# Performance work log

Measured on AMD Instinct MI355X. Metric: run time of the kernel, lower is better.

## Reference

```python
import jax, jax.numpy as jnp
import numpy as np

COMMITMENT_COST = 0.25
NUM_EMBEDDINGS = 512
EMBEDDING_DIM = 64


def setup_inputs() -> dict:
    key = jax.random.key(0)
    k1, k2 = jax.random.split(key)
    inputs = jax.random.normal(k1, (64, EMBEDDING_DIM, 32, 32), dtype=jnp.float32)
    # nn.Embedding init: uniform(-1/K, 1/K)
    emb_w = jax.random.uniform(
        k2, (NUM_EMBEDDINGS, EMBEDDING_DIM), dtype=jnp.float32,
        minval=-1.0 / NUM_EMBEDDINGS, maxval=1.0 / NUM_EMBEDDINGS)
    return {"inputs": inputs, "emb_w": emb_w}


def reference(inputs, emb_w):
    sg = jax.lax.stop_gradient
    # NCHW -> NHWC
    x = jnp.transpose(inputs, (0, 2, 3, 1))          # [B, H, W, D]
    B, H, W, D = x.shape
    flat = x.reshape(-1, D)                          # [N, D]
    dist = (jnp.sum(flat * flat, axis=1, keepdims=True)
            + jnp.sum(emb_w * emb_w, axis=1)
            - 2.0 * jnp.dot(flat, emb_w.T))          # [N, K]
    idx = jnp.argmin(dist, axis=1)                   # [N]
    # one-hot @ emb_w is just a gather
    quantized = emb_w[idx].reshape(B, H, W, D)       # [B, H, W, D]
    e_latent_loss = jnp.mean((sg(quantized) - x) ** 2)
    q_latent_loss = jnp.mean((quantized - sg(x)) ** 2)
    loss = q_latent_loss + COMMITMENT_COST * e_latent_loss
    # straight-through estimator
    quantized_st = x + sg(quantized - x)
    out = jnp.transpose(quantized_st, (0, 3, 1, 2))  # back to NCHW
    return loss, out, idx[:, None]
```

## Files before the change

kernel.cpp:

```cpp
#include <hip/hip_runtime.h>


#define D_     64
#define HW_    1024
#define N_     65536
#define K_     512
#define M_     128
#define CH_    128
#define NCH_   4
#define WCODES 32
#define NDTOT  (N_ * D_)

__global__ __launch_bounds__(256, 2) void vq_fused_kernel(const float* __restrict__ inp,
                                                          const float* __restrict__ emb,
                                                          float* __restrict__ out) {
    __shared__ float ebuf[CH_ * D_];
    __shared__ float ldsn[K_];
    __shared__ float sv[4 * M_];
    __shared__ int   si[4 * M_];
    __shared__ int   fi[M_];

    const int tid  = threadIdx.x;
    const int lane = tid & 63;
    const int w    = tid >> 6;
    const int n0   = blockIdx.x * M_;
    const int b    = n0 >> 10;
    const int hw0  = n0 & 1023;
    const float* xbase = inp + b * (D_ * HW_) + hw0;

#pragma unroll
    for (int i = 0; i < 8; ++i) {
        int q  = i * 256 + tid;
        int d  = q >> 5;
        int pq = q & 31;
        float4 v = *(const float4*)(xbase + d * HW_ + pq * 4);
        *(float4*)(ebuf + d * M_ + pq * 4) = v;
    }

#pragma unroll
    for (int c = 0; c < 2; ++c) {
        const int k = c * 256 + tid;
        const float* e = emb + k * D_;
        float el[64];
#pragma unroll
        for (int q = 0; q < 16; ++q) {
            float4 v = *(const float4*)(e + q * 4);
            el[4 * q + 0] = v.x; el[4 * q + 1] = v.y;
            el[4 * q + 2] = v.z; el[4 * q + 3] = v.w;
        }
        float r[8];
#pragma unroll
        for (int j = 0; j < 8; ++j) r[j] = __fmul_rn(el[j], el[j]);
#pragma unroll
        for (int i = 1; i < 8; ++i)
#pragma unroll
            for (int j = 0; j < 8; ++j)
                r[j] = __fadd_rn(r[j], __fmul_rn(el[i * 8 + j], el[i * 8 + j]));
        ldsn[k] = __fadd_rn(__fadd_rn(__fadd_rn(r[0], r[1]), __fadd_rn(r[2], r[3])),
                            __fadd_rn(__fadd_rn(r[4], r[5]), __fadd_rn(r[6], r[7])));
    }
    __syncthreads();

    float x0[64], x1[64];
#pragma unroll
    for (int d = 0; d < 64; ++d) {
        float2 v = *(const float2*)(ebuf + d * M_ + 2 * lane);
        x0[d] = v.x; x1[d] = v.y;
    }

    float r0[8], r1[8];
#pragma unroll
    for (int j = 0; j < 8; ++j) {
        r0[j] = __fmul_rn(x0[j], x0[j]);
        r1[j] = __fmul_rn(x1[j], x1[j]);
    }
#pragma unroll
    for (int i = 1; i < 8; ++i)
#pragma unroll
        for (int j = 0; j < 8; ++j) {
            r0[j] = __fadd_rn(r0[j], __fmul_rn(x0[i * 8 + j], x0[i * 8 + j]));
            r1[j] = __fadd_rn(r1[j], __fmul_rn(x1[i * 8 + j], x1[i * 8 + j]));
        }
    const float sx0 = __fadd_rn(__fadd_rn(__fadd_rn(r0[0], r0[1]), __fadd_rn(r0[2], r0[3])),
                                __fadd_rn(__fadd_rn(r0[4], r0[5]), __fadd_rn(r0[6], r0[7])));
    const float sx1 = __fadd_rn(__fadd_rn(__fadd_rn(r1[0], r1[1]), __fadd_rn(r1[2], r1[3])),
                                __fadd_rn(__fadd_rn(r1[4], r1[5]), __fadd_rn(r1[6], r1[7])));

    float runv0 = 3.4e38f, runv1 = 3.4e38f;
    int   runi0 = 0,       runi1 = 0;

    for (int c = 0; c < NCH_; ++c) {
        __syncthreads();
        const float4* src = (const float4*)(emb + c * (CH_ * D_));
        float4* dst = (float4*)ebuf;
#pragma unroll
        for (int i = 0; i < 8; ++i) {
            int q = i * 256 + tid;
            dst[q] = src[q];
        }
        __syncthreads();

        const int kbase = c * CH_ + w * WCODES;
        const float* ew = ebuf + (w * WCODES) * D_;
#pragma unroll 2
        for (int kk = 0; kk < WCODES; ++kk) {
            const float* ek = ew + kk * D_;
            const float nk = ldsn[kbase + kk];
            float acc0 = 0.f, acc1 = 0.f;
#pragma unroll
            for (int q = 0; q < 16; ++q) {
                float4 ev = *(const float4*)(ek + q * 4);
                acc0 = fmaf(x0[4 * q + 0], ev.x, acc0); acc1 = fmaf(x1[4 * q + 0], ev.x, acc1);
                acc0 = fmaf(x0[4 * q + 1], ev.y, acc0); acc1 = fmaf(x1[4 * q + 1], ev.y, acc1);
                acc0 = fmaf(x0[4 * q + 2], ev.z, acc0); acc1 = fmaf(x1[4 * q + 2], ev.z, acc1);
                acc0 = fmaf(x0[4 * q + 3], ev.w, acc0); acc1 = fmaf(x1[4 * q + 3], ev.w, acc1);
            }
            float t0 = __fadd_rn(sx0, nk);
            float v0 = __fadd_rn(t0, -2.0f * acc0);
            if (v0 < runv0) { runv0 = v0; runi0 = kbase + kk; }
            float t1 = __fadd_rn(sx1, nk);
            float v1 = __fadd_rn(t1, -2.0f * acc1);
            if (v1 < runv1) { runv1 = v1; runi1 = kbase + kk; }
        }
    }

    {
        const int p0 = 2 * lane, p1 = 2 * lane + 1;
        sv[w * M_ + p0] = runv0; si[w * M_ + p0] = runi0;
        sv[w * M_ + p1] = runv1; si[w * M_ + p1] = runi1;
    }
    __syncthreads();
    if (tid < M_) {
        float bv = 3.4e38f; int bi = 0x7fffffff;
#pragma unroll
        for (int g = 0; g < 4; ++g) {
            float v  = sv[g * M_ + tid];
            int   ii = si[g * M_ + tid];
            if (v < bv || (v == bv && ii < bi)) { bv = v; bi = ii; }
        }
        fi[tid] = bi;
        out[1 + NDTOT + n0 + tid] = (float)bi;
    }
    __syncthreads();

    if (w == 0) {
        const int i0 = fi[2 * lane], i1 = fi[2 * lane + 1];
        const float* e0 = emb + i0 * D_;
        const float* e1 = emb + i1 * D_;
        float local = 0.f;
#pragma unroll
        for (int q = 0; q < 16; ++q) {
            float4 a0 = *(const float4*)(e0 + 4 * q);
            float4 a1 = *(const float4*)(e1 + 4 * q);
            float d00 = a0.x - x0[4 * q + 0]; local = fmaf(d00, d00, local);
            float d01 = a0.y - x0[4 * q + 1]; local = fmaf(d01, d01, local);
            float d02 = a0.z - x0[4 * q + 2]; local = fmaf(d02, d02, local);
            float d03 = a0.w - x0[4 * q + 3]; local = fmaf(d03, d03, local);
            float d10 = a1.x - x1[4 * q + 0]; local = fmaf(d10, d10, local);
            float d11 = a1.y - x1[4 * q + 1]; local = fmaf(d11, d11, local);
            float d12 = a1.z - x1[4 * q + 2]; local = fmaf(d12, d12, local);
            float d13 = a1.w - x1[4 * q + 3]; local = fmaf(d13, d13, local);
        }
#pragma unroll
        for (int off = 32; off > 0; off >>= 1)
            local += __shfl_down(local, off, 64);
        if (lane == 0)
            atomicAdd(out, local * (1.25f / (float)NDTOT));
    }

    float* obase = out + 1 + b * (D_ * HW_) + hw0;
    for (int i = 0; i < 32; ++i) {
        int q = i * 256 + tid;
        int d = q >> 7;
        int p = q & 127;
        obase[d * HW_ + p] = emb[fi[p] * D_ + d];
    }
}

extern "C" void kernel_launch(void* const* d_in, const int* in_sizes, int n_in,
                              void* d_out, int out_size, void* d_ws, size_t ws_size,
                              hipStream_t stream) {
    const float* inp = (const float*)d_in[0];
    const float* emb = (const float*)d_in[1];
    float* out = (float*)d_out;
    (void)d_ws; (void)ws_size;

    hipMemsetAsync(d_out, 0, sizeof(float), stream);
    vq_fused_kernel<<<512, 256, 0, stream>>>(inp, emb, out);
}
```

Measured before the change: 154.1 us.

## Stream codebook through scalar loads instead of LDS staging, drop LDS x tile

The codebook is no longer staged through shared memory in chunks. Each wave now reads its own 128 codes directly into SGPRs with inline s_load_dwordx16 and feeds them as scalar operands to the FMAs, which removes the chunk barriers and LDS reads. Inputs are loaded straight from global memory into registers, skipping the LDS transpose. The output gather is reworked so each thread loads a contiguous half-row of its code with vector loads before the strided stores. The risks are a full lgkmcnt wait on every code with no overlap, heavy SGPR pressure, and the loss of reuse across waves, since each wave now scans a different quarter of the codebook.

```diff
diff --git a/kernel.cpp b/kernel.cpp
--- a/kernel.cpp
+++ b/kernel.cpp
@@ -1,20 +1,19 @@
 #include <hip/hip_runtime.h>
 
+
+typedef float f32x16 __attribute__((ext_vector_type(16)));
 
 #define D_     64
 #define HW_    1024
 #define N_     65536
 #define K_     512
 #define M_     128
-#define CH_    128
-#define NCH_   4
-#define WCODES 32
+#define WCODES 128
 #define NDTOT  (N_ * D_)
 
 __global__ __launch_bounds__(256, 2) void vq_fused_kernel(const float* __restrict__ inp,
                                                           const float* __restrict__ emb,
                                                           float* __restrict__ out) {
-    __shared__ float ebuf[CH_ * D_];
     __shared__ float ldsn[K_];
     __shared__ float sv[4 * M_];
     __shared__ int   si[4 * M_];
@@ -26,16 +25,16 @@
     const int n0   = blockIdx.x * M_;
     const int b    = n0 >> 10;
     const int hw0  = n0 & 1023;
-    const float* xbase = inp + b * (D_ * HW_) + hw0;
 
+    const float* xb = inp + b * (D_ * HW_) + hw0 + 2 * lane;
+    float x0[64], x1[64];
 #pragma unroll
-    for (int i = 0; i < 8; ++i) {
-        int q  = i * 256 + tid;
-        int d  = q >> 5;
-        int pq = q & 31;
-        float4 v = *(const float4*)(xbase + d * HW_ + pq * 4);
-        *(float4*)(ebuf + d * M_ + pq * 4) = v;
+    for (int d = 0; d < 64; ++d) {
+        float2 v = *(const float2*)(xb + d * HW_);
+        x0[d] = v.x; x1[d] = v.y;
     }
+#pragma unroll
+    for (int d = 0; d < 64; ++d) asm volatile("" : "+v"(x0[d]), "+v"(x1[d]));
 
 #pragma unroll
     for (int c = 0; c < 2; ++c) {
@@ -59,14 +58,6 @@
         ldsn[k] = __fadd_rn(__fadd_rn(__fadd_rn(r[0], r[1]), __fadd_rn(r[2], r[3])),
                             __fadd_rn(__fadd_rn(r[4], r[5]), __fadd_rn(r[6], r[7])));
     }
-    __syncthreads();
-
-    float x0[64], x1[64];
-#pragma unroll
-    for (int d = 0; d < 64; ++d) {
-        float2 v = *(const float2*)(ebuf + d * M_ + 2 * lane);
-        x0[d] = v.x; x1[d] = v.y;
-    }
 
     float r0[8], r1[8];
 #pragma unroll
@@ -85,47 +76,56 @@
                                 __fadd_rn(__fadd_rn(r0[4], r0[5]), __fadd_rn(r0[6], r0[7])));
     const float sx1 = __fadd_rn(__fadd_rn(__fadd_rn(r1[0], r1[1]), __fadd_rn(r1[2], r1[3])),
                                 __fadd_rn(__fadd_rn(r1[4], r1[5]), __fadd_rn(r1[6], r1[7])));
+    __syncthreads();
 
     float runv0 = 3.4e38f, runv1 = 3.4e38f;
     int   runi0 = 0,       runi1 = 0;
+    const int kb = __builtin_amdgcn_readfirstlane(w << 7);
+    const float* ew = emb + (size_t)kb * D_;
 
-    for (int c = 0; c < NCH_; ++c) {
-        __syncthreads();
-        const float4* src = (const float4*)(emb + c * (CH_ * D_));
-        float4* dst = (float4*)ebuf;
+    for (int kk = 0; kk < WCODES; ++kk) {
+        const float* ek = ew + kk * D_;
+        f32x16 e0, e1, e2, e3;
+        asm volatile(
+            "s_load_dwordx16 %0, %4, 0x0\n\t"
+            "s_load_dwordx16 %1, %4, 0x40\n\t"
+            "s_load_dwordx16 %2, %4, 0x80\n\t"
+            "s_load_dwordx16 %3, %4, 0xc0\n\t"
+            "s_waitcnt lgkmcnt(0)"
+            : "=s"(e0), "=s"(e1), "=s"(e2), "=s"(e3)
+            : "s"(ek));
+        const float nk = ldsn[kb + kk];
+        float acc0 = 0.f, acc1 = 0.f;
 #pragma unroll
-        for (int i = 0; i < 8; ++i) {
-            int q = i * 256 + tid;
-            dst[q] = src[q];
+        for (int j = 0; j < 16; ++j) {
+            acc0 = fmaf(x0[j], e0[j], acc0);
+            acc1 = fmaf(x1[j], e0[j], acc1);
         }
-        __syncthreads();
-
-        const int kbase = c * CH_ + w * WCODES;
-        const float* ew = ebuf + (w * WCODES) * D_;
-#pragma unroll 2
-        for (int kk = 0; kk < WCODES; ++kk) {
-            const float* ek = ew + kk * D_;
-            const float nk = ldsn[kbase + kk];
-            float acc0 = 0.f, acc1 = 0.f;
 #pragma unroll
-            for (int q = 0; q < 16; ++q) {
-                float4 ev = *(const float4*)(ek + q * 4);
-                acc0 = fmaf(x0[4 * q + 0], ev.x, acc0); acc1 = fmaf(x1[4 * q + 0], ev.x, acc1);
-                acc0 = fmaf(x0[4 * q + 1], ev.y, acc0); acc1 = fmaf(x1[4 * q + 1], ev.y, acc1);
-                acc0 = fmaf(x0[4 * q + 2], ev.z, acc0); acc1 = fmaf(x1[4 * q + 2], ev.z, acc1);
-                acc0 = fmaf(x0[4 * q + 3], ev.w, acc0); acc1 = fmaf(x1[4 * q + 3], ev.w, acc1);
-            }
-            float t0 = __fadd_rn(sx0, nk);
-            float v0 = __fadd_rn(t0, -2.0f * acc0);
-            if (v0 < runv0) { runv0 = v0; runi0 = kbase + kk; }
-            float t1 = __fadd_rn(sx1, nk);
-            float v1 = __fadd_rn(t1, -2.0f * acc1);
-            if (v1 < runv1) { runv1 = v1; runi1 = kbase + kk; }
+        for (int j = 0; j < 16; ++j) {
+            acc0 = fmaf(x0[16 + j], e1[j], acc0);
+            acc1 = fmaf(x1[16 + j], e1[j], acc1);
         }
+#pragma unroll
+        for (int j = 0; j < 16; ++j) {
+            acc0 = fmaf(x0[32 + j], e2[j], acc0);
+            acc1 = fmaf(x1[32 + j], e2[j], acc1);
+        }
+#pragma unroll
+        for (int j = 0; j < 16; ++j) {
+            acc0 = fmaf(x0[48 + j], e3[j], acc0);
+            acc1 = fmaf(x1[48 + j], e3[j], acc1);
+        }
+        float t0 = __fadd_rn(sx0, nk);
+        float v0 = __fadd_rn(t0, -2.0f * acc0);
+        if (v0 < runv0) { runv0 = v0; runi0 = kb + kk; }
+        float t1 = __fadd_rn(sx1, nk);
+        float v1 = __fadd_rn(t1, -2.0f * acc1);
+        if (v1 < runv1) { runv1 = v1; runi1 = kb + kk; }
     }
 
     {
-        const int p0 = 2 * lane, p1 = 2 * lane + 1;
+        const int p0 = 2 * lane, p1 = p0 + 1;
         sv[w * M_ + p0] = runv0; si[w * M_ + p0] = runi0;
         sv[w * M_ + p1] = runv1; si[w * M_ + p1] = runi1;
     }
@@ -145,13 +145,13 @@
 
     if (w == 0) {
         const int i0 = fi[2 * lane], i1 = fi[2 * lane + 1];
-        const float* e0 = emb + i0 * D_;
-        const float* e1 = emb + i1 * D_;
+        const float* e0p = emb + i0 * D_;
+        const float* e1p = emb + i1 * D_;
         float local = 0.f;
 #pragma unroll
         for (int q = 0; q < 16; ++q) {
-            float4 a0 = *(const float4*)(e0 + 4 * q);
-            float4 a1 = *(const float4*)(e1 + 4 * q);
+            float4 a0 = *(const float4*)(e0p + 4 * q);
+            float4 a1 = *(const float4*)(e1p + 4 * q);
             float d00 = a0.x - x0[4 * q + 0]; local = fmaf(d00, d00, local);
             float d01 = a0.y - x0[4 * q + 1]; local = fmaf(d01, d01, local);
             float d02 = a0.z - x0[4 * q + 2]; local = fmaf(d02, d02, local);
@@ -168,12 +168,21 @@
             atomicAdd(out, local * (1.25f / (float)NDTOT));
     }
 
-    float* obase = out + 1 + b * (D_ * HW_) + hw0;
-    for (int i = 0; i < 32; ++i) {
-        int q = i * 256 + tid;
-        int d = q >> 7;
-        int p = q & 127;
-        obase[d * HW_ + p] = emb[fi[p] * D_ + d];
+    {
+        const int p     = tid & 127;
+        const int dhalf = tid >> 7;
+        const float* er = emb + fi[p] * D_ + dhalf * 32;
+        float ev[32];
+#pragma unroll
+        for (int q = 0; q < 8; ++q) {
+            float4 v = *(const float4*)(er + 4 * q);
+            ev[4 * q + 0] = v.x; ev[4 * q + 1] = v.y;
+            ev[4 * q + 2] = v.z; ev[4 * q + 3] = v.w;
+        }
+        float* ob = out + 1 + b * (D_ * HW_) + hw0 + p;
+#pragma unroll
+        for (int dd = 0; dd < 32; ++dd)
+            ob[(dhalf * 32 + dd) * HW_] = ev[dd];
     }
 }
 
```

New measurement: 138.1 us. 1.12x faster.

## Register-tile the distance GEMM with a 16x8 outer-product per thread

Applied to the files above, without the earlier changes.

Replaces the per-thread two-point dot-product loop with a register-blocked outer product: each thread accumulates 16 points by 8 codes over D, reading x and transposed codebook tiles from padded LDS. The codebook is loaded into LDS in two 256-code transposed chunks instead of four 128-code chunks, and the argmin reduction now merges 32 partial columns per point. The epilogue loss and output write are spread across all 256 threads, with a shared-memory partial sum. The cost is a large LDS footprint and about 128 accumulator registers per thread, so occupancy drops to one block per SIMD group (launch_bounds 256,1).

```diff
diff --git a/kernel.cpp b/kernel.cpp
--- a/kernel.cpp
+++ b/kernel.cpp
@@ -6,23 +6,25 @@
 #define N_     65536
 #define K_     512
 #define M_     128
-#define CH_    128
-#define NCH_   4
-#define WCODES 32
 #define NDTOT  (N_ * D_)
-
-__global__ __launch_bounds__(256, 2) void vq_fused_kernel(const float* __restrict__ inp,
+#define XP     160
+#define EP     256
+
+__global__ __launch_bounds__(256, 1) void vq_fused_kernel(const float* __restrict__ inp,
                                                           const float* __restrict__ emb,
                                                           float* __restrict__ out) {
-    __shared__ float ebuf[CH_ * D_];
+    __shared__ float ldsx[D_ * XP];
+    __shared__ float ldse[D_ * EP];
     __shared__ float ldsn[K_];
-    __shared__ float sv[4 * M_];
-    __shared__ int   si[4 * M_];
+    __shared__ float sxs[M_];
     __shared__ int   fi[M_];
+    __shared__ float psum[256];
 
     const int tid  = threadIdx.x;
     const int lane = tid & 63;
     const int w    = tid >> 6;
+    const int pg   = lane & 7;
+    const int kg   = lane >> 3;
     const int n0   = blockIdx.x * M_;
     const int b    = n0 >> 10;
     const int hw0  = n0 & 1023;
@@ -30,13 +32,12 @@
 
 #pragma unroll
     for (int i = 0; i < 8; ++i) {
-        int q  = i * 256 + tid;
-        int d  = q >> 5;
+        int q = i * 256 + tid;
+        int d = q >> 5;
         int pq = q & 31;
         float4 v = *(const float4*)(xbase + d * HW_ + pq * 4);
-        *(float4*)(ebuf + d * M_ + pq * 4) = v;
-    }
-
+        *(float4*)(ldsx + d * XP + (pq >> 2) * 20 + (pq & 3) * 4) = v;
+    }
 #pragma unroll
     for (int c = 0; c < 2; ++c) {
         const int k = c * 256 + tid;
@@ -59,83 +60,131 @@
         ldsn[k] = __fadd_rn(__fadd_rn(__fadd_rn(r[0], r[1]), __fadd_rn(r[2], r[3])),
                             __fadd_rn(__fadd_rn(r[4], r[5]), __fadd_rn(r[6], r[7])));
     }
-    __syncthreads();
-
-    float x0[64], x1[64];
-#pragma unroll
-    for (int d = 0; d < 64; ++d) {
-        float2 v = *(const float2*)(ebuf + d * M_ + 2 * lane);
-        x0[d] = v.x; x1[d] = v.y;
-    }
-
-    float r0[8], r1[8];
-#pragma unroll
-    for (int j = 0; j < 8; ++j) {
-        r0[j] = __fmul_rn(x0[j], x0[j]);
-        r1[j] = __fmul_rn(x1[j], x1[j]);
-    }
-#pragma unroll
-    for (int i = 1; i < 8; ++i)
+#pragma unroll
+    for (int i = 0; i < 16; ++i) {
+        float4 v = *(const float4*)(emb + tid * D_ + i * 4);
+        ldse[(i * 4 + 0) * EP + tid] = v.x;
+        ldse[(i * 4 + 1) * EP + tid] = v.y;
+        ldse[(i * 4 + 2) * EP + tid] = v.z;
+        ldse[(i * 4 + 3) * EP + tid] = v.w;
+    }
+    __syncthreads();
+
+    if (tid < M_) {
+        const int xb2 = (tid >> 4) * 20 + (tid & 15);
+        float r[8];
 #pragma unroll
         for (int j = 0; j < 8; ++j) {
-            r0[j] = __fadd_rn(r0[j], __fmul_rn(x0[i * 8 + j], x0[i * 8 + j]));
-            r1[j] = __fadd_rn(r1[j], __fmul_rn(x1[i * 8 + j], x1[i * 8 + j]));
-        }
-    const float sx0 = __fadd_rn(__fadd_rn(__fadd_rn(r0[0], r0[1]), __fadd_rn(r0[2], r0[3])),
-                                __fadd_rn(__fadd_rn(r0[4], r0[5]), __fadd_rn(r0[6], r0[7])));
-    const float sx1 = __fadd_rn(__fadd_rn(__fadd_rn(r1[0], r1[1]), __fadd_rn(r1[2], r1[3])),
-                                __fadd_rn(__fadd_rn(r1[4], r1[5]), __fadd_rn(r1[6], r1[7])));
-
-    float runv0 = 3.4e38f, runv1 = 3.4e38f;
-    int   runi0 = 0,       runi1 = 0;
-
-    for (int c = 0; c < NCH_; ++c) {
-        __syncthreads();
-        const float4* src = (const float4*)(emb + c * (CH_ * D_));
-        float4* dst = (float4*)ebuf;
-#pragma unroll
-        for (int i = 0; i < 8; ++i) {
-            int q = i * 256 + tid;
-            dst[q] = src[q];
-        }
-        __syncthreads();
-
-        const int kbase = c * CH_ + w * WCODES;
-        const float* ew = ebuf + (w * WCODES) * D_;
-#pragma unroll 2
-        for (int kk = 0; kk < WCODES; ++kk) {
-            const float* ek = ew + kk * D_;
-            const float nk = ldsn[kbase + kk];
-            float acc0 = 0.f, acc1 = 0.f;
-#pragma unroll
-            for (int q = 0; q < 16; ++q) {
-                float4 ev = *(const float4*)(ek + q * 4);
-                acc0 = fmaf(x0[4 * q + 0], ev.x, acc0); acc1 = fmaf(x1[4 * q + 0], ev.x, acc1);
-                acc0 = fmaf(x0[4 * q + 1], ev.y, acc0); acc1 = fmaf(x1[4 * q + 1], ev.y, acc1);
-                acc0 = fmaf(x0[4 * q + 2], ev.z, acc0); acc1 = fmaf(x1[4 * q + 2], ev.z, acc1);
-                acc0 = fmaf(x0[4 * q + 3], ev.w, acc0); acc1 = fmaf(x1[4 * q + 3], ev.w, acc1);
+            float v = ldsx[j * XP + xb2];
+            r[j] = __fmul_rn(v, v);
+        }
+#pragma unroll
+        for (int i = 1; i < 8; ++i)
+#pragma unroll
+            for (int j = 0; j < 8; ++j) {
+                float v = ldsx[(i * 8 + j) * XP + xb2];
+                r[j] = __fadd_rn(r[j], __fmul_rn(v, v));
             }
-            float t0 = __fadd_rn(sx0, nk);
-            float v0 = __fadd_rn(t0, -2.0f * acc0);
-            if (v0 < runv0) { runv0 = v0; runi0 = kbase + kk; }
-            float t1 = __fadd_rn(sx1, nk);
-            float v1 = __fadd_rn(t1, -2.0f * acc1);
-            if (v1 < runv1) { runv1 = v1; runi1 = kbase + kk; }
-        }
-    }
-
+        sxs[tid] = __fadd_rn(__fadd_rn(__fadd_rn(r[0], r[1]), __fadd_rn(r[2], r[3])),
+                             __fadd_rn(__fadd_rn(r[4], r[5]), __fadd_rn(r[6], r[7])));
+    }
+    __syncthreads();
+
+    float sxp[16];
     {
-        const int p0 = 2 * lane, p1 = 2 * lane + 1;
-        sv[w * M_ + p0] = runv0; si[w * M_ + p0] = runi0;
-        sv[w * M_ + p1] = runv1; si[w * M_ + p1] = runi1;
+        float4 s0 = *(const float4*)(sxs + pg * 16);
+        float4 s1 = *(const float4*)(sxs + pg * 16 + 4);
+        float4 s2 = *(const float4*)(sxs + pg * 16 + 8);
+        float4 s3 = *(const float4*)(sxs + pg * 16 + 12);
+        sxp[0]=s0.x; sxp[1]=s0.y; sxp[2]=s0.z; sxp[3]=s0.w;
+        sxp[4]=s1.x; sxp[5]=s1.y; sxp[6]=s1.z; sxp[7]=s1.w;
+        sxp[8]=s2.x; sxp[9]=s2.y; sxp[10]=s2.z; sxp[11]=s2.w;
+        sxp[12]=s3.x; sxp[13]=s3.y; sxp[14]=s3.z; sxp[15]=s3.w;
+    }
+    float runv[16];
+    int   runi[16];
+#pragma unroll
+    for (int j = 0; j < 16; ++j) { runv[j] = 3.4e38f; runi[j] = 0; }
+
+#pragma unroll 1
+    for (int c = 0; c < 2; ++c) {
+        if (c) {
+            __syncthreads();
+#pragma unroll
+            for (int i = 0; i < 16; ++i) {
+                float4 v = *(const float4*)(emb + (256 + tid) * D_ + i * 4);
+                ldse[(i * 4 + 0) * EP + tid] = v.x;
+                ldse[(i * 4 + 1) * EP + tid] = v.y;
+                ldse[(i * 4 + 2) * EP + tid] = v.z;
+                ldse[(i * 4 + 3) * EP + tid] = v.w;
+            }
+            __syncthreads();
+        }
+        float nk[8];
+        {
+            float4 na = *(const float4*)(ldsn + c * 256 + w * 64 + kg * 8);
+            float4 nb = *(const float4*)(ldsn + c * 256 + w * 64 + kg * 8 + 4);
+            nk[0]=na.x; nk[1]=na.y; nk[2]=na.z; nk[3]=na.w;
+            nk[4]=nb.x; nk[5]=nb.y; nk[6]=nb.z; nk[7]=nb.w;
+        }
+        float acc[16][8];
+#pragma unroll
+        for (int j = 0; j < 16; ++j)
+#pragma unroll
+            for (int q = 0; q < 8; ++q) acc[j][q] = 0.f;
+
+        const float* xcol = ldsx + pg * 20;
+        const float* ecol = ldse + (w << 6) + (kg << 3);
+#pragma unroll 4
+        for (int d = 0; d < 64; ++d) {
+            const float* xr = xcol + d * XP;
+            float4 xa = *(const float4*)(xr);
+            float4 xb4 = *(const float4*)(xr + 4);
+            float4 xc4 = *(const float4*)(xr + 8);
+            float4 xd4 = *(const float4*)(xr + 12);
+            const float* er = ecol + d * EP;
+            float4 ea = *(const float4*)(er);
+            float4 eb = *(const float4*)(er + 4);
+            float xv[16] = {xa.x, xa.y, xa.z, xa.w, xb4.x, xb4.y, xb4.z, xb4.w,
+                            xc4.x, xc4.y, xc4.z, xc4.w, xd4.x, xd4.y, xd4.z, xd4.w};
+            float ev[8]  = {ea.x, ea.y, ea.z, ea.w, eb.x, eb.y, eb.z, eb.w};
+#pragma unroll
+            for (int j = 0; j < 16; ++j)
+#pragma unroll
+                for (int q = 0; q < 8; ++q)
+                    acc[j][q] = fmaf(xv[j], ev[q], acc[j][q]);
+        }
+
+        const int kidx0 = c * 256 + w * 64 + kg * 8;
+#pragma unroll
+        for (int j = 0; j < 16; ++j) {
+            float sx = sxp[j];
+#pragma unroll
+            for (int q = 0; q < 8; ++q) {
+                float t = __fadd_rn(sx, nk[q]);
+                float v = __fadd_rn(t, -2.0f * acc[j][q]);
+                if (v < runv[j]) { runv[j] = v; runi[j] = kidx0 + q; }
+            }
+        }
+    }
+
+    __syncthreads();
+    float* mv = ldse;
+    int*   mi = (int*)(ldse + 128 * 33);
+    const int col = w * 8 + kg;
+#pragma unroll
+    for (int j = 0; j < 16; ++j) {
+        int p = pg * 16 + j;
+        mv[p * 33 + col] = runv[j];
+        mi[p * 33 + col] = runi[j];
     }
     __syncthreads();
     if (tid < M_) {
         float bv = 3.4e38f; int bi = 0x7fffffff;
 #pragma unroll
-        for (int g = 0; g < 4; ++g) {
-            float v  = sv[g * M_ + tid];
-            int   ii = si[g * M_ + tid];
+        for (int g = 0; g < 32; ++g) {
+            float v  = mv[tid * 33 + g];
+            int   ii = mi[tid * 33 + g];
             if (v < bv || (v == bv && ii < bi)) { bv = v; bi = ii; }
         }
         fi[tid] = bi;
@@ -143,37 +192,37 @@
     }
     __syncthreads();
 
-    if (w == 0) {
-        const int i0 = fi[2 * lane], i1 = fi[2 * lane + 1];
-        const float* e0 = emb + i0 * D_;
-        const float* e1 = emb + i1 * D_;
+    {
+        const int p  = tid & 127;
+        const int dh = tid >> 7;
+        const float* er2 = emb + fi[p] * D_ + dh * 32;
+        float ev2[32];
+#pragma unroll
+        for (int q = 0; q < 8; ++q) {
+            float4 v = *(const float4*)(er2 + 4 * q);
+            ev2[4 * q + 0] = v.x; ev2[4 * q + 1] = v.y;
+            ev2[4 * q + 2] = v.z; ev2[4 * q + 3] = v.w;
+        }
+        float* ob = out + 1 + b * (D_ * HW_) + hw0 + p;
+        const int xb2 = (p >> 4) * 20 + (p & 15);
         float local = 0.f;
 #pragma unroll
-        for (int q = 0; q < 16; ++q) {
-            float4 a0 = *(const float4*)(e0 + 4 * q);
-            float4 a1 = *(const float4*)(e1 + 4 * q);
-            float d00 = a0.x - x0[4 * q + 0]; local = fmaf(d00, d00, local);
-            float d01 = a0.y - x0[4 * q + 1]; local = fmaf(d01, d01, local);
-            float d02 = a0.z - x0[4 * q + 2]; local = fmaf(d02, d02, local);
-            float d03 = a0.w - x0[4 * q + 3]; local = fmaf(d03, d03, local);
-            float d10 = a1.x - x1[4 * q + 0]; local = fmaf(d10, d10, local);
-            float d11 = a1.y - x1[4 * q + 1]; local = fmaf(d11, d11, local);
-            float d12 = a1.z - x1[4 * q + 2]; local = fmaf(d12, d12, local);
-            float d13 = a1.w - x1[4 * q + 3]; local = fmaf(d13, d13, local);
-        }
+        for (int dd = 0; dd < 32; ++dd) {
+            float xv = ldsx[(dh * 32 + dd) * XP + xb2];
+            float df = ev2[dd] - xv;
+            local = fmaf(df, df, local);
+            ob[(dh * 32 + dd) * HW_] = ev2[dd];
+        }
+        psum[tid] = local;
+    }
+    __syncthreads();
+    if (tid < 64) {
+        float s = psum[tid] + psum[tid + 64] + psum[tid + 128] + psum[tid + 192];
 #pragma unroll
         for (int off = 32; off > 0; off >>= 1)
-            local += __shfl_down(local, off, 64);
-        if (lane == 0)
-            atomicAdd(out, local * (1.25f / (float)NDTOT));
-    }
-
-    float* obase = out + 1 + b * (D_ * HW_) + hw0;
-    for (int i = 0; i < 32; ++i) {
-        int q = i * 256 + tid;
-        int d = q >> 7;
-        int p = q & 127;
-        obase[d * HW_ + p] = emb[fi[p] * D_ + d];
+            s += __shfl_down(s, off, 64);
+        if (tid == 0)
+            atomicAdd(out, s * (1.25f / (float)NDTOT));
     }
 }
 
```

Result: no change. 153.5 us (-0.4%).
